# Optimization experiments

Measured on AMD Instinct MI355X. Metric: run time of the kernel, lower is better.

Reference implementation:

```python
import jax, jax.numpy as jnp
import numpy as np

NBINS = 256

def _equalize_flat(flat):
    # flat: [N, P] int32 pixel values in [0,255], N = B*C channels, P = H*W pixels
    N, P = flat.shape
    hist = jax.vmap(lambda v: jnp.bincount(v, length=NBINS))(flat)  # [N, 256]
    bins = jnp.arange(NBINS, dtype=jnp.int32)
    # last nonzero bin value per channel (PIL: drop last nonzero entry from the step sum)
    last_idx = jnp.max(jnp.where(hist != 0, bins[None, :], -1), axis=1)  # [N]
    last_val = jnp.take_along_axis(hist, last_idx[:, None], axis=1)[:, 0]  # [N]
    step = (P - last_val) // 255  # [N] integer floor div
    safe_step = jnp.maximum(step, 1)
    cs = jnp.cumsum(hist, axis=1)  # [N, 256]
    lut = (cs + (step // 2)[:, None]) // safe_step[:, None]
    # pad left with 0, drop last, clamp to [0,255]
    lut = jnp.concatenate([jnp.zeros((N, 1), lut.dtype), lut[:, :-1]], axis=1)
    lut = jnp.clip(lut, 0, 255)
    eq = jnp.take_along_axis(lut, flat, axis=1)  # [N, P]
    # channels with step==0 pass through unchanged
    return jnp.where((step == 0)[:, None], flat, eq)


def setup_inputs() -> dict:
    key = jax.random.key(0)
    img = jax.random.randint(key, (64, 3, 512, 512), 0, 256).astype(jnp.float32)
    return {"img": img}


def reference(img) -> jnp.ndarray:
    B, C, H, W = img.shape
    flat = img.astype(jnp.int32).reshape(B * C, H * W)
    out = _equalize_flat(flat)
    return out.reshape(B, C, H, W).astype(img.dtype)
```

## Files before the change

kernel.cpp:

```cpp
#include <hip/hip_runtime.h>


#define NBINS 256
#define BPC 32

typedef float vfloat4 __attribute__((ext_vector_type(4)));

__global__ __launch_bounds__(256) void eq_hist_kernel(
    const float* __restrict__ in, unsigned int* __restrict__ phist,
    int P, int bpc) {
    __shared__ unsigned int lh[NBINS * 32];
    const int t = threadIdx.x;
    const int copy = t & 31;

    for (int i = t; i < NBINS * 32; i += 256) lh[i] = 0u;
    __syncthreads();

    const int chan = blockIdx.x / bpc;
    const int blk  = blockIdx.x % bpc;
    const int chunk = P / bpc;
    const size_t base = (size_t)chan * P + (size_t)blk * chunk;
    const float4* vin = (const float4*)(in + base);
    const int nvec = chunk / 4;

    for (int i = t; i < nvec; i += 256) {
        float4 v = vin[i];
        int ix = min(max((int)v.x, 0), 255);
        int iy = min(max((int)v.y, 0), 255);
        int iz = min(max((int)v.z, 0), 255);
        int iw = min(max((int)v.w, 0), 255);
        atomicAdd(&lh[ix * 32 + copy], 1u);
        atomicAdd(&lh[iy * 32 + copy], 1u);
        atomicAdd(&lh[iz * 32 + copy], 1u);
        atomicAdd(&lh[iw * 32 + copy], 1u);
    }
    __syncthreads();

    unsigned int s = 0;
    #pragma unroll
    for (int c = 0; c < 32; ++c)
        s += lh[t * 32 + ((t + c) & 31)];
    phist[(size_t)blockIdx.x * NBINS + t] = s;
}

__global__ __launch_bounds__(256) void eq_lut_kernel(
    const unsigned int* __restrict__ phist, float* __restrict__ glut,
    int P, int bpc) {
    __shared__ unsigned int s[NBINS];
    __shared__ int sidx[NBINS];
    const int t = threadIdx.x;
    const int chan = blockIdx.x;

    unsigned int h = 0;
    const unsigned int* pbase = phist + (size_t)chan * bpc * NBINS;
    for (int b = 0; b < bpc; ++b) h += pbase[b * NBINS + t];
    s[t] = h;
    sidx[t] = (h != 0u) ? t : -1;
    __syncthreads();

    for (int off = 128; off > 0; off >>= 1) {
        if (t < off) sidx[t] = max(sidx[t], sidx[t + off]);
        __syncthreads();
    }
    const int last_idx = sidx[0];
    const unsigned int last_val = s[last_idx];
    const int step = (P - (int)last_val) / 255;

    for (int off = 1; off < NBINS; off <<= 1) {
        unsigned int val = (t >= off) ? s[t - off] : 0u;
        __syncthreads();
        s[t] += val;
        __syncthreads();
    }

    float lv;
    if (step == 0) {
        lv = (float)t;
    } else {
        int cs_prev = (t == 0) ? 0 : (int)s[t - 1];
        int l = (cs_prev + (step >> 1)) / step;
        l = min(max(l, 0), 255);
        lv = (float)l;
    }
    glut[chan * NBINS + t] = lv;
}

__global__ __launch_bounds__(256) void eq_apply_kernel(
    const float* __restrict__ in, const float* __restrict__ glut,
    float* __restrict__ out, int P, int bpc) {
    __shared__ float slut[NBINS * 32];
    const int t = threadIdx.x;
    const int copy = t & 31;
    const int chan = blockIdx.x / bpc;
    const int blk  = blockIdx.x % bpc;

    const float lv = glut[chan * NBINS + t];
    #pragma unroll
    for (int c = 0; c < 32; ++c)
        slut[t * 32 + ((t + c) & 31)] = lv;
    __syncthreads();

    const int chunk = P / bpc;
    const size_t base = (size_t)chan * P + (size_t)blk * chunk;
    const float4* vin = (const float4*)(in + base);
    vfloat4* vout = (vfloat4*)(out + base);
    const int nvec = chunk / 4;

    for (int i = t; i < nvec; i += 256) {
        float4 v = vin[i];
        vfloat4 r;
        r.x = slut[min(max((int)v.x, 0), 255) * 32 + copy];
        r.y = slut[min(max((int)v.y, 0), 255) * 32 + copy];
        r.z = slut[min(max((int)v.z, 0), 255) * 32 + copy];
        r.w = slut[min(max((int)v.w, 0), 255) * 32 + copy];
        __builtin_nontemporal_store(r, &vout[i]);
    }
}

extern "C" void kernel_launch(void* const* d_in, const int* in_sizes, int n_in,
                              void* d_out, int out_size, void* d_ws, size_t ws_size,
                              hipStream_t stream) {
    const float* img = (const float*)d_in[0];
    float* out = (float*)d_out;

    const int P = 512 * 512;
    const int total = in_sizes[0];
    const int N = total / P;

    unsigned int* phist = (unsigned int*)d_ws;
    float* glut = (float*)((char*)d_ws +
                           (size_t)N * BPC * NBINS * sizeof(unsigned int));

    eq_hist_kernel<<<N * BPC, 256, 0, stream>>>(img, phist, P, BPC);
    eq_lut_kernel<<<N, 256, 0, stream>>>(phist, glut, P, BPC);
    eq_apply_kernel<<<N * BPC, 256, 0, stream>>>(img, glut, out, P, BPC);
}
```

Before: 367.7 us.

## Pack clamped pixels to bytes in histogram pass and fuse LUT with apply

The histogram kernel now also writes each pixel as a packed 8-bit index. The LUT build is merged into the apply kernel, which reads the packed bytes instead of the float image. This cuts the second full read of the float input to a quarter-size read, and removes one kernel launch and the LUT round trip. The trade-offs are that the LUT is recomputed per block, and that blocks per channel drop from 32 to 4, which reduces parallelism.

```diff
diff --git a/kernel.cpp b/kernel.cpp
--- a/kernel.cpp
+++ b/kernel.cpp
@@ -2,28 +2,31 @@
 
 
 #define NBINS 256
-#define BPC 32
+#define BPC 4
+#define CHUNK 65536
+#define NVEC (CHUNK / 4)
 
 typedef float vfloat4 __attribute__((ext_vector_type(4)));
 
-__global__ __launch_bounds__(256) void eq_hist_kernel(
-    const float* __restrict__ in, unsigned int* __restrict__ phist,
-    int P, int bpc) {
+__global__ __launch_bounds__(256) void eq_hist_pack_kernel(
+    const float* __restrict__ in, unsigned int* __restrict__ pack,
+    unsigned int* __restrict__ phist) {
     __shared__ unsigned int lh[NBINS * 32];
     const int t = threadIdx.x;
     const int copy = t & 31;
+    const int chan = blockIdx.x >> 2;
+    const int blk  = blockIdx.x & 3;
 
     for (int i = t; i < NBINS * 32; i += 256) lh[i] = 0u;
     __syncthreads();
 
-    const int chan = blockIdx.x / bpc;
-    const int blk  = blockIdx.x % bpc;
-    const int chunk = P / bpc;
-    const size_t base = (size_t)chan * P + (size_t)blk * chunk;
-    const float4* vin = (const float4*)(in + base);
-    const int nvec = chunk / 4;
+    const size_t basev = ((size_t)chan * (size_t)(CHUNK * BPC) +
+                          (size_t)blk * CHUNK) >> 2;
+    const float4* vin = (const float4*)in + basev;
+    unsigned int* pout = pack + basev;
 
-    for (int i = t; i < nvec; i += 256) {
+    #pragma unroll 4
+    for (int i = t; i < NVEC; i += 256) {
         float4 v = vin[i];
         int ix = min(max((int)v.x, 0), 255);
         int iy = min(max((int)v.y, 0), 255);
@@ -33,27 +36,32 @@
         atomicAdd(&lh[iy * 32 + copy], 1u);
         atomicAdd(&lh[iz * 32 + copy], 1u);
         atomicAdd(&lh[iw * 32 + copy], 1u);
+        pout[i] = (unsigned)ix | ((unsigned)iy << 8) |
+                  ((unsigned)iz << 16) | ((unsigned)iw << 24);
     }
     __syncthreads();
 
     unsigned int s = 0;
     #pragma unroll
-    for (int c = 0; c < 32; ++c)
-        s += lh[t * 32 + ((t + c) & 31)];
+    for (int c = 0; c < 32; ++c) s += lh[t * 32 + ((t + c) & 31)];
     phist[(size_t)blockIdx.x * NBINS + t] = s;
 }
 
-__global__ __launch_bounds__(256) void eq_lut_kernel(
-    const unsigned int* __restrict__ phist, float* __restrict__ glut,
-    int P, int bpc) {
+__global__ __launch_bounds__(256) void eq_lut_apply_kernel(
+    const unsigned int* __restrict__ pack, const unsigned int* __restrict__ phist,
+    float* __restrict__ out, int P) {
+    __shared__ float slut[NBINS * 32];
     __shared__ unsigned int s[NBINS];
     __shared__ int sidx[NBINS];
     const int t = threadIdx.x;
-    const int chan = blockIdx.x;
+    const int copy = t & 31;
+    const int chan = blockIdx.x >> 2;
+    const int blk  = blockIdx.x & 3;
 
     unsigned int h = 0;
-    const unsigned int* pbase = phist + (size_t)chan * bpc * NBINS;
-    for (int b = 0; b < bpc; ++b) h += pbase[b * NBINS + t];
+    const unsigned int* pb = phist + (size_t)chan * BPC * NBINS;
+    #pragma unroll
+    for (int b = 0; b < BPC; ++b) h += pb[b * NBINS + t];
     s[t] = h;
     sidx[t] = (h != 0u) ? t : -1;
     __syncthreads();
@@ -63,13 +71,13 @@
         __syncthreads();
     }
     const int last_idx = sidx[0];
-    const unsigned int last_val = s[last_idx];
-    const int step = (P - (int)last_val) / 255;
+    const int last_val = (int)s[last_idx];
+    const int step = (P - last_val) / 255;
 
     for (int off = 1; off < NBINS; off <<= 1) {
-        unsigned int val = (t >= off) ? s[t - off] : 0u;
+        unsigned int v = (t >= off) ? s[t - off] : 0u;
         __syncthreads();
-        s[t] += val;
+        s[t] += v;
         __syncthreads();
     }
 
@@ -77,42 +85,28 @@
     if (step == 0) {
         lv = (float)t;
     } else {
-        int cs_prev = (t == 0) ? 0 : (int)s[t - 1];
-        int l = (cs_prev + (step >> 1)) / step;
-        l = min(max(l, 0), 255);
-        lv = (float)l;
+        int csp = (t == 0) ? 0 : (int)s[t - 1];
+        int l = (csp + (step >> 1)) / step;
+        lv = (float)min(max(l, 0), 255);
     }
-    glut[chan * NBINS + t] = lv;
-}
-
-__global__ __launch_bounds__(256) void eq_apply_kernel(
-    const float* __restrict__ in, const float* __restrict__ glut,
-    float* __restrict__ out, int P, int bpc) {
-    __shared__ float slut[NBINS * 32];
-    const int t = threadIdx.x;
-    const int copy = t & 31;
-    const int chan = blockIdx.x / bpc;
-    const int blk  = blockIdx.x % bpc;
-
-    const float lv = glut[chan * NBINS + t];
     #pragma unroll
     for (int c = 0; c < 32; ++c)
         slut[t * 32 + ((t + c) & 31)] = lv;
     __syncthreads();
 
-    const int chunk = P / bpc;
-    const size_t base = (size_t)chan * P + (size_t)blk * chunk;
-    const float4* vin = (const float4*)(in + base);
-    vfloat4* vout = (vfloat4*)(out + base);
-    const int nvec = chunk / 4;
+    const size_t basev = ((size_t)chan * (size_t)(CHUNK * BPC) +
+                          (size_t)blk * CHUNK) >> 2;
+    const unsigned int* pin = pack + basev;
+    vfloat4* vout = (vfloat4*)out + basev;
 
-    for (int i = t; i < nvec; i += 256) {
-        float4 v = vin[i];
+    #pragma unroll 4
+    for (int i = t; i < NVEC; i += 256) {
+        unsigned int p = pin[i];
         vfloat4 r;
-        r.x = slut[min(max((int)v.x, 0), 255) * 32 + copy];
-        r.y = slut[min(max((int)v.y, 0), 255) * 32 + copy];
-        r.z = slut[min(max((int)v.z, 0), 255) * 32 + copy];
-        r.w = slut[min(max((int)v.w, 0), 255) * 32 + copy];
+        r.x = slut[(p & 255u) * 32 + copy];
+        r.y = slut[((p >> 8) & 255u) * 32 + copy];
+        r.z = slut[((p >> 16) & 255u) * 32 + copy];
+        r.w = slut[(p >> 24) * 32 + copy];
         __builtin_nontemporal_store(r, &vout[i]);
     }
 }
@@ -127,11 +121,9 @@
     const int total = in_sizes[0];
     const int N = total / P;
 
-    unsigned int* phist = (unsigned int*)d_ws;
-    float* glut = (float*)((char*)d_ws +
-                           (size_t)N * BPC * NBINS * sizeof(unsigned int));
+    unsigned int* pack  = (unsigned int*)d_ws;
+    unsigned int* phist = (unsigned int*)((char*)d_ws + (size_t)total);
 
-    eq_hist_kernel<<<N * BPC, 256, 0, stream>>>(img, phist, P, BPC);
-    eq_lut_kernel<<<N, 256, 0, stream>>>(phist, glut, P, BPC);
-    eq_apply_kernel<<<N * BPC, 256, 0, stream>>>(img, glut, out, P, BPC);
+    eq_hist_pack_kernel<<<N * BPC, 256, 0, stream>>>(img, pack, phist);
+    eq_lut_apply_kernel<<<N * BPC, 256, 0, stream>>>(pack, phist, out, P);
 }
```

Result: faster. 349.1 us (-5.1%).
